# Performance work log

Measured on AMD Instinct MI355X. Metric: run time of the kernel, lower is better.

Reference implementation:

```python
import jax, jax.numpy as jnp
import numpy as np

N, E, G = 50000, 800000, 500
F_IN, H_DIM, L, NH, HD, OUT = 74, 256, 4, 8, 32, 1
SLOPE, EPS = 0.2, 1e-5


def setup_inputs() -> dict:
    key = jax.random.key(0)
    ks = jax.random.split(key, 24)
    rn = lambda k, s, sc: jax.random.normal(k, s, jnp.float32) * sc
    inp = {
        "x": jax.random.normal(ks[0], (N, F_IN), jnp.float32),
        "edge_index": jax.random.randint(ks[1], (2, E), 0, N),
        "batch": jnp.sort(jax.random.randint(ks[2], (N,), 0, G)),
        "in_w": rn(ks[3], (F_IN, H_DIM), 1.0 / np.sqrt(F_IN)),
        "in_b": jnp.zeros((H_DIM,), jnp.float32),
        "wl": rn(ks[4], (L, H_DIM, H_DIM), 1.0 / np.sqrt(H_DIM)),
        "wl_b": jnp.zeros((L, H_DIM), jnp.float32),
        "wr": rn(ks[5], (L, H_DIM, H_DIM), 1.0 / np.sqrt(H_DIM)),
        "wr_b": jnp.zeros((L, H_DIM), jnp.float32),
        "att": rn(ks[6], (L, NH, HD), 1.0 / np.sqrt(HD)),
        "gat_b": jnp.zeros((L, H_DIM), jnp.float32),
        "ln_g": jnp.ones((L, H_DIM), jnp.float32),
        "ln_b": jnp.zeros((L, H_DIM), jnp.float32),
        "out_w": rn(ks[7], (H_DIM, H_DIM), 1.0 / np.sqrt(H_DIM)),
        "out_b": jnp.zeros((H_DIM,), jnp.float32),
        "p1_w": rn(ks[8], (H_DIM, H_DIM // 2), 1.0 / np.sqrt(H_DIM)),
        "p1_b": jnp.zeros((H_DIM // 2,), jnp.float32),
        "bn1_g": jnp.ones((H_DIM // 2,), jnp.float32),
        "bn1_b": jnp.zeros((H_DIM // 2,), jnp.float32),
        "p2_w": rn(ks[9], (H_DIM // 2, H_DIM // 4), 1.0 / np.sqrt(H_DIM // 2)),
        "p2_b": jnp.zeros((H_DIM // 4,), jnp.float32),
        "bn2_g": jnp.ones((H_DIM // 4,), jnp.float32),
        "bn2_b": jnp.zeros((H_DIM // 4,), jnp.float32),
        "p3_w": rn(ks[10], (H_DIM // 4, OUT), 1.0 / np.sqrt(H_DIM // 4)),
        "p3_b": jnp.zeros((OUT,), jnp.float32),
    }
    return inp


def _layer_norm(x, g, b):
    m = x.mean(-1, keepdims=True)
    v = ((x - m) ** 2).mean(-1, keepdims=True)
    return (x - m) * jax.lax.rsqrt(v + EPS) * g + b


def _batch_norm(x, g, b):
    m = x.mean(0)
    v = ((x - m) ** 2).mean(0)
    return (x - m) * jax.lax.rsqrt(v + EPS) * g + b


def _gatv2(h, src, dst, wl, wl_b, wr, wr_b, att, bias, n):
    xl = (h @ wl + wl_b).reshape(n, NH, HD)  # source transform
    xr = (h @ wr + wr_b).reshape(n, NH, HD)  # target transform
    e = jax.nn.leaky_relu(xl[src] + xr[dst], SLOPE)      # [E, H, D]
    score = jnp.einsum('ehd,hd->eh', e, att)             # [E, H]
    smax = jax.ops.segment_max(score, dst, num_segments=n)
    num = jnp.exp(score - smax[dst])
    den = jax.ops.segment_sum(num, dst, num_segments=n)
    alpha = num / (den[dst] + 1e-16)                     # segment softmax per dst
    out = jax.ops.segment_sum(xl[src] * alpha[:, :, None], dst, num_segments=n)
    return out.reshape(n, NH * HD) + bias


def reference(x, edge_index, batch, in_w, in_b, wl, wl_b, wr, wr_b, att, gat_b,
              ln_g, ln_b, out_w, out_b, p1_w, p1_b, bn1_g, bn1_b,
              p2_w, p2_b, bn2_g, bn2_b, p3_w, p3_b):
    n = x.shape[0]
    loops = jnp.arange(n)
    src = jnp.concatenate([edge_index[0], loops])  # add self-loops (PyG default)
    dst = jnp.concatenate([edge_index[1], loops])
    h = x @ in_w + in_b
    for i in range(L):
        res = h
        g = _gatv2(h, src, dst, wl[i], wl_b[i], wr[i], wr_b[i], att[i], gat_b[i], n)
        if i > 0:
            g = g + res
        h = jax.nn.relu(_layer_norm(g, ln_g[i], ln_b[i]))
    h = h @ out_w + out_b
    cnt = jax.ops.segment_sum(jnp.ones((n,), h.dtype), batch, num_segments=G)
    gr = jax.ops.segment_sum(h, batch, num_segments=G) / jnp.maximum(cnt, 1.0)[:, None]
    z = jax.nn.relu(_batch_norm(gr @ p1_w + p1_b, bn1_g, bn1_b))
    z = jax.nn.relu(_batch_norm(z @ p2_w + p2_b, bn2_g, bn2_b))
    return z @ p3_w + p3_b
```

## Files before the change

kernel.cpp:

```cpp
#include <hip/hip_runtime.h>
#include <hip/hip_bf16.h>

#define F_IN   74
#define HDIM   256
#define NHEAD  8
#define HEADD  32
#define NLAYER 4
#define SLOPE  0.2f
#define EPSN   1e-5f

typedef __attribute__((ext_vector_type(8))) short bf16x8;
typedef __attribute__((ext_vector_type(4))) float f32x4;

__device__ __forceinline__ float bf2f(unsigned short u){
  union { unsigned int i; float f; } x; x.i = ((unsigned int)u) << 16; return x.f;
}
__device__ __forceinline__ unsigned short f2bf(float f){
  union { float f; unsigned int i; } x; x.f = f;
  unsigned int u = x.i;
  return (unsigned short)((u + 0x7FFFu + ((u >> 16) & 1u)) >> 16);
}

#define GLOAD16(g, s) __builtin_amdgcn_global_load_lds( \
  (const __attribute__((address_space(1))) void*)(g), \
  (__attribute__((address_space(3))) void*)(s), 16, 0, 0)

__global__ void k_hist(const int* __restrict__ dst, int* __restrict__ deg, int e){
  int i = blockIdx.x * 256 + threadIdx.x;
  if (i < e) atomicAdd(&deg[dst[i]], 1);
}

__global__ __launch_bounds__(256) void k_scan1(const int* __restrict__ deg,
    int* __restrict__ rowp, int* __restrict__ bsum, int n){
  __shared__ int wsum[4];
  const int tid = threadIdx.x, lane = tid & 63, wid = tid >> 6;
  const int i = blockIdx.x * 256 + tid;
  int v = (i < n) ? (deg[i] + 1) : 0;
  int xv = v;
  #pragma unroll
  for (int off = 1; off < 64; off <<= 1){
    int t = __shfl_up(xv, off);
    if (lane >= off) xv += t;
  }
  if (lane == 63) wsum[wid] = xv;
  __syncthreads();
  int woff = 0, total = 0;
  #pragma unroll
  for (int w = 0; w < 4; ++w){
    int s = wsum[w];
    total += s;
    if (w < wid) woff += s;
  }
  if (i < n) rowp[i] = woff + xv - v;
  if (tid == 0) bsum[blockIdx.x] = total;
}
__global__ __launch_bounds__(256) void k_scan2(const int* __restrict__ bsum,
    int* __restrict__ boff, int nb){
  __shared__ int wsum[4];
  const int tid = threadIdx.x, lane = tid & 63, wid = tid >> 6;
  int v = (tid < nb) ? bsum[tid] : 0;
  int xv = v;
  #pragma unroll
  for (int off = 1; off < 64; off <<= 1){
    int t = __shfl_up(xv, off);
    if (lane >= off) xv += t;
  }
  if (lane == 63) wsum[wid] = xv;
  __syncthreads();
  int woff = 0, total = 0;
  #pragma unroll
  for (int w = 0; w < 4; ++w){
    int s = wsum[w];
    total += s;
    if (w < wid) woff += s;
  }
  if (tid <= nb) boff[tid] = woff + xv - v;
  if (tid == 0) boff[nb] = total;
}
__global__ void k_scan3(int* __restrict__ rowp, const int* __restrict__ boff,
                        int n, int nb){
  int i = blockIdx.x * 256 + threadIdx.x;
  if (i < n) rowp[i] += boff[blockIdx.x];
  if (i == 0) rowp[n] = boff[nb];
}

__global__ void k_copy(const int* __restrict__ a, int* __restrict__ b, int n){
  int i = blockIdx.x * 256 + threadIdx.x;
  if (i < n) b[i] = a[i];
}
__global__ void k_fill(const int* __restrict__ src, const int* __restrict__ dst,
                       int* __restrict__ cur, int* __restrict__ csr, int e){
  int i = blockIdx.x * 256 + threadIdx.x;
  if (i < e){
    int p = atomicAdd(&cur[dst[i]], 1);
    csr[p] = src[i];
  }
}
__global__ void k_fillself(int* __restrict__ cur, int* __restrict__ csr, int n){
  int i = blockIdx.x * 256 + threadIdx.x;
  if (i < n){
    int p = atomicAdd(&cur[i], 1);
    csr[p] = i;
  }
}

__global__ __launch_bounds__(256) void k_inproj(
    const float* __restrict__ x, const float* __restrict__ w,
    const float* __restrict__ b, unsigned short* __restrict__ h, int n)
{
  __shared__ float xs[32 * F_IN];
  const int n0 = blockIdx.x * 32;
  const int tid = threadIdx.x;
  const int maxidx = n * F_IN;
  for (int idx = tid; idx < 32 * F_IN; idx += 256){
    int gidx = n0 * F_IN + idx;
    xs[idx] = (gidx < maxidx) ? x[gidx] : 0.f;
  }
  __syncthreads();
  float acc[32];
  #pragma unroll
  for (int i = 0; i < 32; ++i) acc[i] = 0.f;
  for (int k = 0; k < F_IN; ++k){
    float wk = w[k * HDIM + tid];
    #pragma unroll
    for (int i = 0; i < 32; ++i) acc[i] += xs[i * F_IN + k] * wk;
  }
  float bb = b[tid];
  #pragma unroll
  for (int i = 0; i < 32; ++i){
    int r = n0 + i;
    if (r < n) h[(size_t)r * HDIM + tid] = f2bf(acc[i] + bb);
  }
}

__global__ __launch_bounds__(256) void k_wconv(const float* __restrict__ W,
    unsigned short* __restrict__ Wt, size_t mat_stride){
  __shared__ float tile[32][33];
  const int mat = blockIdx.z;
  const float* Wm = W + (size_t)mat * HDIM * HDIM;
  unsigned short* Wo = Wt + (size_t)mat * mat_stride;
  const int c0 = blockIdx.x * 32, r0 = blockIdx.y * 32;
  const int tx = threadIdx.x & 31, ty = threadIdx.x >> 5;
  #pragma unroll
  for (int i = 0; i < 32; i += 8)
    tile[ty + i][tx] = Wm[(size_t)(r0 + ty + i) * HDIM + c0 + tx];
  __syncthreads();
  #pragma unroll
  for (int i = 0; i < 32; i += 8)
    Wo[(size_t)(c0 + ty + i) * HDIM + r0 + tx] = f2bf(tile[tx][ty + i]);
}

__global__ void k_bcat(const float* __restrict__ wl_b, const float* __restrict__ wr_b,
                       float* __restrict__ bc){
  int i = blockIdx.x * 256 + threadIdx.x;
  if (i >= NLAYER * 512) return;
  int layer = i >> 9, c = i & 511;
  bc[i] = (c < 256) ? wl_b[layer * 256 + c] : wr_b[layer * 256 + (c - 256)];
}

__global__ __launch_bounds__(256) void k_gemm_mfma(
    const unsigned short* __restrict__ A, const unsigned short* __restrict__ Wt,
    const float* __restrict__ bias, unsigned short* __restrict__ C, int M, int ldc)
{
  __shared__ unsigned short As[2][128 * 64];
  __shared__ unsigned short Bs[2][128 * 64];
  const int tid = threadIdx.x;
  const int l   = tid & 63;
  const int w   = tid >> 6;
  const int wm  = w >> 1, wn = w & 1;
  const int row0 = blockIdx.x * 128;
  const int col0 = blockIdx.y * 128;

  const int srow   = l >> 3;
  const int schunk = l & 7;

  f32x4 acc[4][4];
  #pragma unroll
  for (int i = 0; i < 4; ++i)
    #pragma unroll
    for (int j = 0; j < 4; ++j) acc[i][j] = (f32x4){0.f, 0.f, 0.f, 0.f};

  auto stage = [&](int buf, int k0){
    #pragma unroll
    for (int i = 0; i < 4; ++i){
      const int rloc = w * 32 + i * 8 + srow;
      const int sw   = (schunk ^ (rloc & 7)) * 16;
      int ra = row0 + rloc; if (ra > M - 1) ra = M - 1;
      const char* srcA = (const char*)(A + (size_t)ra * HDIM + k0) + sw;
      GLOAD16(srcA, &As[buf][(w * 32 + i * 8) * 64]);
      const char* srcB = (const char*)(Wt + (size_t)(col0 + rloc) * HDIM + k0) + sw;
      GLOAD16(srcB, &Bs[buf][(w * 32 + i * 8) * 64]);
    }
  };

  auto compute = [&](int buf){
    #pragma unroll
    for (int kk = 0; kk < 2; ++kk){
      bf16x8 af[4], bfr[4];
      #pragma unroll
      for (int mi = 0; mi < 4; ++mi){
        const int row = wm * 64 + mi * 16 + (l & 15);
        const int t   = (kk * 4 + (l >> 4)) ^ (row & 7);
        af[mi] = *(const bf16x8*)((const char*)&As[buf][0] + row * 128 + t * 16);
      }
      #pragma unroll
      for (int ni = 0; ni < 4; ++ni){
        const int nn = wn * 64 + ni * 16 + (l & 15);
        const int t  = (kk * 4 + (l >> 4)) ^ (nn & 7);
        bfr[ni] = *(const bf16x8*)((const char*)&Bs[buf][0] + nn * 128 + t * 16);
      }
      #pragma unroll
      for (int mi = 0; mi < 4; ++mi)
        #pragma unroll
        for (int ni = 0; ni < 4; ++ni)
          acc[mi][ni] = __builtin_amdgcn_mfma_f32_16x16x32_bf16(
              af[mi], bfr[ni], acc[mi][ni], 0, 0, 0);
    }
  };

  stage(0, 0);
  int cur = 0;
  #pragma unroll
  for (int t = 0; t < 4; ++t){
    if (t < 3){
      stage(cur ^ 1, (t + 1) * 64);
      asm volatile("s_waitcnt vmcnt(8)" ::: "memory");
    } else {
      asm volatile("s_waitcnt vmcnt(0)" ::: "memory");
    }
    __builtin_amdgcn_s_barrier();
    compute(cur);
    asm volatile("" ::: "memory");
    __builtin_amdgcn_s_barrier();
    cur ^= 1;
  }

  #pragma unroll
  for (int mi = 0; mi < 4; ++mi){
    #pragma unroll
    for (int ni = 0; ni < 4; ++ni){
      const int col = col0 + wn * 64 + ni * 16 + (l & 15);
      const float bv = bias[col];
      #pragma unroll
      for (int r = 0; r < 4; ++r){
        const int row = row0 + wm * 64 + mi * 16 + (l >> 4) * 4 + r;
        if (row < M) C[(size_t)row * ldc + col] = f2bf(acc[mi][ni][r] + bv);
      }
    }
  }
}

__global__ __launch_bounds__(256) void k_gat(
    const unsigned short* __restrict__ xlr,
    const int* __restrict__ rp, const int* __restrict__ csr,
    const float* __restrict__ att, const float* __restrict__ gb,
    const float* __restrict__ lg, const float* __restrict__ lb,
    const unsigned short* __restrict__ hold, unsigned short* __restrict__ hnew,
    int n, int use_res)
{
  const int node = blockIdx.x * 4 + (threadIdx.x >> 6);
  if (node >= n) return;
  const int lane = threadIdx.x & 63;
  const int elem = lane << 2;
  const int head = lane >> 3;
  float4 attv = *(const float4*)(att + head * HEADD + (elem & 31));
  ushort4 ur = *(const ushort4*)(xlr + (size_t)node * 512 + 256 + elem);
  const float xr0 = bf2f(ur.x), xr1 = bf2f(ur.y), xr2 = bf2f(ur.z), xr3 = bf2f(ur.w);

  auto scoref = [&](ushort4 u)->float{
    float t0 = bf2f(u.x) + xr0; t0 = t0 > 0.f ? t0 : SLOPE * t0;
    float t1 = bf2f(u.y) + xr1; t1 = t1 > 0.f ? t1 : SLOPE * t1;
    float t2 = bf2f(u.z) + xr2; t2 = t2 > 0.f ? t2 : SLOPE * t2;
    float t3 = bf2f(u.w) + xr3; t3 = t3 > 0.f ? t3 : SLOPE * t3;
    float p = attv.x * t0 + attv.y * t1 + attv.z * t2 + attv.w * t3;
    p += __shfl_xor(p, 1);
    p += __shfl_xor(p, 2);
    p += __shfl_xor(p, 4);
    return p;
  };

  float m = -1e30f, l = 0.f, a0 = 0.f, a1 = 0.f, a2 = 0.f, a3 = 0.f;
  const int e0 = rp[node], e1 = rp[node + 1];
  int e = e0;
  for (; e + 4 <= e1; e += 4){
    int s0 = csr[e], s1 = csr[e + 1], s2 = csr[e + 2], s3 = csr[e + 3];
    ushort4 u0 = *(const ushort4*)(xlr + (size_t)s0 * 512 + elem);
    ushort4 u1 = *(const ushort4*)(xlr + (size_t)s1 * 512 + elem);
    ushort4 u2 = *(const ushort4*)(xlr + (size_t)s2 * 512 + elem);
    ushort4 u3 = *(const ushort4*)(xlr + (size_t)s3 * 512 + elem);
    float p0 = scoref(u0), p1 = scoref(u1), p2 = scoref(u2), p3 = scoref(u3);
    float mn = fmaxf(m, fmaxf(fmaxf(p0, p1), fmaxf(p2, p3)));
    float sc = __expf(m - mn);
    float q0 = __expf(p0 - mn), q1 = __expf(p1 - mn);
    float q2 = __expf(p2 - mn), q3 = __expf(p3 - mn);
    l = l * sc + q0 + q1 + q2 + q3;
    a0 = a0 * sc + q0 * bf2f(u0.x) + q1 * bf2f(u1.x) + q2 * bf2f(u2.x) + q3 * bf2f(u3.x);
    a1 = a1 * sc + q0 * bf2f(u0.y) + q1 * bf2f(u1.y) + q2 * bf2f(u2.y) + q3 * bf2f(u3.y);
    a2 = a2 * sc + q0 * bf2f(u0.z) + q1 * bf2f(u1.z) + q2 * bf2f(u2.z) + q3 * bf2f(u3.z);
    a3 = a3 * sc + q0 * bf2f(u0.w) + q1 * bf2f(u1.w) + q2 * bf2f(u2.w) + q3 * bf2f(u3.w);
    m = mn;
  }
  for (; e < e1; ++e){
    int s = csr[e];
    ushort4 u = *(const ushort4*)(xlr + (size_t)s * 512 + elem);
    float p = scoref(u);
    float mn = fmaxf(m, p);
    float sc = __expf(m - mn);
    float pe = __expf(p - mn);
    l  = l * sc + pe;
    a0 = a0 * sc + pe * bf2f(u.x);
    a1 = a1 * sc + pe * bf2f(u.y);
    a2 = a2 * sc + pe * bf2f(u.z);
    a3 = a3 * sc + pe * bf2f(u.w);
    m = mn;
  }
  const float inv = 1.f / l;
  const size_t base = (size_t)node * HDIM + elem;
  float f0 = a0 * inv + gb[elem + 0];
  float f1 = a1 * inv + gb[elem + 1];
  float f2 = a2 * inv + gb[elem + 2];
  float f3 = a3 * inv + gb[elem + 3];
  if (use_res){
    ushort4 hv = *(const ushort4*)(hold + base);
    f0 += bf2f(hv.x); f1 += bf2f(hv.y); f2 += bf2f(hv.z); f3 += bf2f(hv.w);
  }
  float s = f0 + f1 + f2 + f3;
  #pragma unroll
  for (int off = 1; off < 64; off <<= 1) s += __shfl_xor(s, off);
  const float mean = s * (1.f / HDIM);
  float d0 = f0 - mean, d1 = f1 - mean, d2 = f2 - mean, d3 = f3 - mean;
  float q = d0 * d0 + d1 * d1 + d2 * d2 + d3 * d3;
  #pragma unroll
  for (int off = 1; off < 64; off <<= 1) q += __shfl_xor(q, off);
  const float rs = rsqrtf(q * (1.f / HDIM) + EPSN);
  float o0 = d0 * rs * lg[elem + 0] + lb[elem + 0]; o0 = o0 > 0.f ? o0 : 0.f;
  float o1 = d1 * rs * lg[elem + 1] + lb[elem + 1]; o1 = o1 > 0.f ? o1 : 0.f;
  float o2 = d2 * rs * lg[elem + 2] + lb[elem + 2]; o2 = o2 > 0.f ? o2 : 0.f;
  float o3 = d3 * rs * lg[elem + 3] + lb[elem + 3]; o3 = o3 > 0.f ? o3 : 0.f;
  ushort4 st; st.x = f2bf(o0); st.y = f2bf(o1); st.z = f2bf(o2); st.w = f2bf(o3);
  *(ushort4*)(hnew + base) = st;
}

__global__ __launch_bounds__(256) void k_pool2(
    const unsigned short* __restrict__ ho, const int* __restrict__ batch,
    float* __restrict__ gr, int n)
{
  const int g = blockIdx.x;
  int lo = 0, hi = n;
  while (lo < hi){ int mid = (lo + hi) >> 1; if (batch[mid] < g) lo = mid + 1; else hi = mid; }
  const int s = lo;
  hi = n;
  while (lo < hi){ int mid = (lo + hi) >> 1; if (batch[mid] < g + 1) lo = mid + 1; else hi = mid; }
  const int e = lo;
  const int j = threadIdx.x;
  float acc = 0.f;
  for (int i = s; i < e; ++i) acc += bf2f(ho[(size_t)i * HDIM + j]);
  int c = e - s; if (c < 1) c = 1;
  gr[(size_t)g * HDIM + j] = acc / (float)c;
}

__global__ void k_fc(const float* __restrict__ in, const float* __restrict__ w,
                     const float* __restrict__ b, float* __restrict__ out,
                     int kin, int kout){
  __shared__ float s[256];
  int g = blockIdx.x, j = threadIdx.x;
  for (int k = j; k < kin; k += blockDim.x) s[k] = in[(size_t)g * kin + k];
  __syncthreads();
  float a = b[j];
  for (int k = 0; k < kin; ++k) a = fmaf(s[k], w[k * kout + j], a);
  out[(size_t)g * kout + j] = a;
}
__global__ __launch_bounds__(256) void k_bnstats(const float* __restrict__ z,
    float* __restrict__ mean, float* __restrict__ rstd, int g_, int c_){
  int c = blockIdx.x;
  float s = 0.f, s2 = 0.f;
  for (int r = threadIdx.x; r < g_; r += 256){
    float v = z[(size_t)r * c_ + c];
    s += v; s2 += v * v;
  }
  #pragma unroll
  for (int off = 1; off < 64; off <<= 1){ s += __shfl_xor(s, off); s2 += __shfl_xor(s2, off); }
  __shared__ float sw[4], sw2[4];
  int lane = threadIdx.x & 63, wid = threadIdx.x >> 6;
  if (lane == 0){ sw[wid] = s; sw2[wid] = s2; }
  __syncthreads();
  if (threadIdx.x == 0){
    float ts = sw[0] + sw[1] + sw[2] + sw[3];
    float ts2 = sw2[0] + sw2[1] + sw2[2] + sw2[3];
    float mm = ts / g_;
    float vv = ts2 / g_ - mm * mm;
    mean[c] = mm; rstd[c] = rsqrtf(vv + EPSN);
  }
}
__global__ void k_bnrelu(float* __restrict__ z, const float* __restrict__ mean,
                         const float* __restrict__ rstd, const float* __restrict__ g,
                         const float* __restrict__ b, int total, int c_){
  int i = blockIdx.x * 256 + threadIdx.x;
  if (i < total){
    int c = i & (c_ - 1);
    float v = (z[i] - mean[c]) * rstd[c] * g[c] + b[c];
    z[i] = v > 0.f ? v : 0.f;
  }
}
__global__ __launch_bounds__(256) void k_out(const float* __restrict__ z,
    const float* __restrict__ w, const float* __restrict__ b,
    float* __restrict__ out, int g_){
  int g = blockIdx.x * 4 + (threadIdx.x >> 6);
  if (g >= g_) return;
  int lane = threadIdx.x & 63;
  float v = z[(size_t)g * 64 + lane] * w[lane];
  #pragma unroll
  for (int off = 1; off < 64; off <<= 1) v += __shfl_xor(v, off);
  if (lane == 0) out[g] = v + b[0];
}

extern "C" void kernel_launch(void* const* d_in, const int* in_sizes, int n_in,
                              void* d_out, int out_size, void* d_ws, size_t ws_size,
                              hipStream_t stream)
{
  const float* x     = (const float*)d_in[0];
  const int*   ei    = (const int*)  d_in[1];
  const int*   batch = (const int*)  d_in[2];
  const float* in_w  = (const float*)d_in[3];
  const float* in_b  = (const float*)d_in[4];
  const float* wl    = (const float*)d_in[5];
  const float* wl_b  = (const float*)d_in[6];
  const float* wr    = (const float*)d_in[7];
  const float* wr_b  = (const float*)d_in[8];
  const float* att   = (const float*)d_in[9];
  const float* gat_b = (const float*)d_in[10];
  const float* ln_g  = (const float*)d_in[11];
  const float* ln_b  = (const float*)d_in[12];
  const float* out_w = (const float*)d_in[13];
  const float* out_b = (const float*)d_in[14];
  const float* p1_w  = (const float*)d_in[15];
  const float* p1_b  = (const float*)d_in[16];
  const float* bn1_g = (const float*)d_in[17];
  const float* bn1_b = (const float*)d_in[18];
  const float* p2_w  = (const float*)d_in[19];
  const float* p2_b  = (const float*)d_in[20];
  const float* bn2_g = (const float*)d_in[21];
  const float* bn2_b = (const float*)d_in[22];
  const float* p3_w  = (const float*)d_in[23];
  const float* p3_b  = (const float*)d_in[24];

  const int n = in_sizes[0] / F_IN;
  const int e = in_sizes[1] / 2;
  const int g = out_size;
  const int nb = (n + 255) / 256;

  char* p = (char*)d_ws;
  auto take = [&](size_t bytes)->char*{
    char* q = p; p += ((bytes + 255) & ~(size_t)255); return q;
  };
  unsigned short* hA   = (unsigned short*)take((size_t)n * HDIM * 2);
  unsigned short* hB   = (unsigned short*)take((size_t)n * HDIM * 2);
  unsigned short* xlr  = (unsigned short*)take((size_t)n * 512 * 2);
  unsigned short* WtLR = (unsigned short*)take((size_t)NLAYER * 512 * HDIM * 2);
  unsigned short* WtO  = (unsigned short*)take((size_t)HDIM * HDIM * 2);
  float* bconc = (float*)take((size_t)NLAYER * 512 * 4);
  int*   deg   = (int*)take((size_t)n * 4);
  int*   rowp  = (int*)take((size_t)(n + 1) * 4);
  int*   cur   = (int*)take((size_t)n * 4);
  int*   csr   = (int*)take((size_t)(e + n) * 4);
  int*   bsum  = (int*)take((size_t)(nb + 1) * 4);
  int*   boff  = (int*)take((size_t)(nb + 1) * 4);
  float* gr    = (float*)take((size_t)g * HDIM * 4);
  float* z1    = (float*)take((size_t)g * 128 * 4);
  float* z2    = (float*)take((size_t)g * 64 * 4);
  float* mean1 = (float*)take(128 * 4);
  float* rstd1 = (float*)take(128 * 4);
  float* mean2 = (float*)take(64 * 4);
  float* rstd2 = (float*)take(64 * 4);
  (void)ws_size; (void)n_in;

  hipMemsetAsync(deg, 0, (size_t)n * 4, stream);
  k_hist<<<(e + 255) / 256, 256, 0, stream>>>(ei + e, deg, e);
  k_scan1<<<nb, 256, 0, stream>>>(deg, rowp, bsum, n);
  k_scan2<<<1, 256, 0, stream>>>(bsum, boff, nb);
  k_scan3<<<nb, 256, 0, stream>>>(rowp, boff, n, nb);
  k_copy<<<(n + 255) / 256, 256, 0, stream>>>(rowp, cur, n);
  k_fill<<<(e + 255) / 256, 256, 0, stream>>>(ei, ei + e, cur, csr, e);
  k_fillself<<<(n + 255) / 256, 256, 0, stream>>>(cur, csr, n);

  k_wconv<<<dim3(8, 8, 4), 256, 0, stream>>>(wl, WtLR, (size_t)512 * HDIM);
  k_wconv<<<dim3(8, 8, 4), 256, 0, stream>>>(wr, WtLR + (size_t)256 * HDIM, (size_t)512 * HDIM);
  k_wconv<<<dim3(8, 8, 1), 256, 0, stream>>>(out_w, WtO, (size_t)HDIM * HDIM);
  k_bcat<<<(NLAYER * 512 + 255) / 256, 256, 0, stream>>>(wl_b, wr_b, bconc);

  k_inproj<<<(n + 31) / 32, 256, 0, stream>>>(x, in_w, in_b, hA, n);

  unsigned short* hcur = hA;
  unsigned short* hnext = hB;
  for (int i = 0; i < NLAYER; ++i){
    k_gemm_mfma<<<dim3((n + 127) / 128, 4), 256, 0, stream>>>(
        hcur, WtLR + (size_t)i * 512 * HDIM, bconc + i * 512, xlr, n, 512);
    k_gat<<<(n + 3) / 4, 256, 0, stream>>>(xlr, rowp, csr,
        att + (size_t)i * NHEAD * HEADD, gat_b + i * HDIM,
        ln_g + i * HDIM, ln_b + i * HDIM, hcur, hnext, n, i > 0 ? 1 : 0);
    unsigned short* t = hcur; hcur = hnext; hnext = t;
  }
  k_gemm_mfma<<<dim3((n + 127) / 128, 2), 256, 0, stream>>>(
      hcur, WtO, out_b, hnext, n, HDIM);

  k_pool2<<<g, 256, 0, stream>>>(hnext, batch, gr, n);

  k_fc<<<g, 128, 0, stream>>>(gr, p1_w, p1_b, z1, HDIM, 128);
  k_bnstats<<<128, 256, 0, stream>>>(z1, mean1, rstd1, g, 128);
  k_bnrelu<<<(g * 128 + 255) / 256, 256, 0, stream>>>(z1, mean1, rstd1, bn1_g, bn1_b, g * 128, 128);
  k_fc<<<g, 64, 0, stream>>>(z1, p2_w, p2_b, z2, 128, 64);
  k_bnstats<<<64, 256, 0, stream>>>(z2, mean2, rstd2, g, 64);
  k_bnrelu<<<(g * 64 + 255) / 256, 256, 0, stream>>>(z2, mean2, rstd2, bn2_g, bn2_b, g * 64, 64);
  k_out<<<(g + 3) / 4, 256, 0, stream>>>(z2, p3_w, p3_b, (float*)d_out, g);
}
```

Baseline: 758.0 us.

## Use MFMA for input projection, drop softmax max tracking, fuse scan copy

The input projection now runs on bf16 MFMA instructions. The input and weight are first converted to bf16 and padded to K=96, with the padded input stored in the xlr scratch buffer. The GAT aggregation drops the online-softmax running maximum and rescaling and just accumulates exp(score), which saves several exp and multiply operations per edge. That risks overflow when scores are large. The separate k_copy of rowp into cur is folded into k_scan3, removing one launch.

```diff
diff --git a/kernel.cpp b/kernel.cpp
--- a/kernel.cpp
+++ b/kernel.cpp
@@ -2,6 +2,7 @@
 #include <hip/hip_bf16.h>
 
 #define F_IN   74
+#define KPAD   96
 #define HDIM   256
 #define NHEAD  8
 #define HEADD  32
@@ -77,17 +78,17 @@
   if (tid <= nb) boff[tid] = woff + xv - v;
   if (tid == 0) boff[nb] = total;
 }
-__global__ void k_scan3(int* __restrict__ rowp, const int* __restrict__ boff,
-                        int n, int nb){
+__global__ void k_scan3(int* __restrict__ rowp, int* __restrict__ cur,
+                        const int* __restrict__ boff, int n, int nb){
   int i = blockIdx.x * 256 + threadIdx.x;
-  if (i < n) rowp[i] += boff[blockIdx.x];
+  if (i < n){
+    int v = rowp[i] + boff[blockIdx.x];
+    rowp[i] = v;
+    cur[i] = v;
+  }
   if (i == 0) rowp[n] = boff[nb];
 }
 
-__global__ void k_copy(const int* __restrict__ a, int* __restrict__ b, int n){
-  int i = blockIdx.x * 256 + threadIdx.x;
-  if (i < n) b[i] = a[i];
-}
 __global__ void k_fill(const int* __restrict__ src, const int* __restrict__ dst,
                        int* __restrict__ cur, int* __restrict__ csr, int e){
   int i = blockIdx.x * 256 + threadIdx.x;
@@ -104,32 +105,77 @@
   }
 }
 
-__global__ __launch_bounds__(256) void k_inproj(
-    const float* __restrict__ x, const float* __restrict__ w,
-    const float* __restrict__ b, unsigned short* __restrict__ h, int n)
+__global__ void k_xconv(const float* __restrict__ x, unsigned short* __restrict__ xb,
+                        int n){
+  int idx = blockIdx.x * 256 + threadIdx.x;
+  int total = n * KPAD;
+  if (idx >= total) return;
+  int row = idx / KPAD;
+  int k = idx - row * KPAD;
+  float v = (k < F_IN) ? x[(size_t)row * F_IN + k] : 0.f;
+  xb[idx] = f2bf(v);
+}
+
+__global__ void k_wconv_in(const float* __restrict__ w, unsigned short* __restrict__ Wt){
+  int idx = blockIdx.x * 256 + threadIdx.x;
+  if (idx >= HDIM * KPAD) return;
+  int c = idx / KPAD;
+  int k = idx - c * KPAD;
+  float v = (k < F_IN) ? w[(size_t)k * HDIM + c] : 0.f;
+  Wt[idx] = f2bf(v);
+}
+
+__global__ __launch_bounds__(256) void k_inproj_mfma(
+    const unsigned short* __restrict__ xb, const unsigned short* __restrict__ Wt,
+    const float* __restrict__ bias, unsigned short* __restrict__ C, int M)
 {
-  __shared__ float xs[32 * F_IN];
-  const int n0 = blockIdx.x * 32;
-  const int tid = threadIdx.x;
-  const int maxidx = n * F_IN;
-  for (int idx = tid; idx < 32 * F_IN; idx += 256){
-    int gidx = n0 * F_IN + idx;
-    xs[idx] = (gidx < maxidx) ? x[gidx] : 0.f;
-  }
-  __syncthreads();
-  float acc[32];
-  #pragma unroll
-  for (int i = 0; i < 32; ++i) acc[i] = 0.f;
-  for (int k = 0; k < F_IN; ++k){
-    float wk = w[k * HDIM + tid];
-    #pragma unroll
-    for (int i = 0; i < 32; ++i) acc[i] += xs[i * F_IN + k] * wk;
-  }
-  float bb = b[tid];
-  #pragma unroll
-  for (int i = 0; i < 32; ++i){
-    int r = n0 + i;
-    if (r < n) h[(size_t)r * HDIM + tid] = f2bf(acc[i] + bb);
+  const int l = threadIdx.x & 63;
+  const int w = threadIdx.x >> 6;
+  const int wm = w >> 1, wn = w & 1;
+  const int row0 = blockIdx.x * 128;
+  const int col0 = blockIdx.y * 128;
+
+  f32x4 acc[4][4];
+  #pragma unroll
+  for (int i = 0; i < 4; ++i)
+    #pragma unroll
+    for (int j = 0; j < 4; ++j) acc[i][j] = (f32x4){0.f, 0.f, 0.f, 0.f};
+
+  #pragma unroll
+  for (int kk = 0; kk < 3; ++kk){
+    const int kof = kk * 32 + (l >> 4) * 8;
+    bf16x8 af[4], bfr[4];
+    #pragma unroll
+    for (int mi = 0; mi < 4; ++mi){
+      int row = row0 + wm * 64 + mi * 16 + (l & 15);
+      if (row > M - 1) row = M - 1;
+      af[mi] = *(const bf16x8*)(xb + (size_t)row * KPAD + kof);
+    }
+    #pragma unroll
+    for (int ni = 0; ni < 4; ++ni){
+      const int col = col0 + wn * 64 + ni * 16 + (l & 15);
+      bfr[ni] = *(const bf16x8*)(Wt + (size_t)col * KPAD + kof);
+    }
+    #pragma unroll
+    for (int mi = 0; mi < 4; ++mi)
+      #pragma unroll
+      for (int ni = 0; ni < 4; ++ni)
+        acc[mi][ni] = __builtin_amdgcn_mfma_f32_16x16x32_bf16(
+            af[mi], bfr[ni], acc[mi][ni], 0, 0, 0);
+  }
+
+  #pragma unroll
+  for (int mi = 0; mi < 4; ++mi){
+    #pragma unroll
+    for (int ni = 0; ni < 4; ++ni){
+      const int col = col0 + wn * 64 + ni * 16 + (l & 15);
+      const float bv = bias[col];
+      #pragma unroll
+      for (int r = 0; r < 4; ++r){
+        const int row = row0 + wm * 64 + mi * 16 + (l >> 4) * 4 + r;
+        if (row < M) C[(size_t)row * HDIM + col] = f2bf(acc[mi][ni][r] + bv);
+      }
+    }
   }
 }
 
@@ -279,7 +325,7 @@
     return p;
   };
 
-  float m = -1e30f, l = 0.f, a0 = 0.f, a1 = 0.f, a2 = 0.f, a3 = 0.f;
+  float l = 0.f, a0 = 0.f, a1 = 0.f, a2 = 0.f, a3 = 0.f;
   const int e0 = rp[node], e1 = rp[node + 1];
   int e = e0;
   for (; e + 4 <= e1; e += 4){
@@ -288,31 +334,23 @@
     ushort4 u1 = *(const ushort4*)(xlr + (size_t)s1 * 512 + elem);
     ushort4 u2 = *(const ushort4*)(xlr + (size_t)s2 * 512 + elem);
     ushort4 u3 = *(const ushort4*)(xlr + (size_t)s3 * 512 + elem);
-    float p0 = scoref(u0), p1 = scoref(u1), p2 = scoref(u2), p3 = scoref(u3);
-    float mn = fmaxf(m, fmaxf(fmaxf(p0, p1), fmaxf(p2, p3)));
-    float sc = __expf(m - mn);
-    float q0 = __expf(p0 - mn), q1 = __expf(p1 - mn);
-    float q2 = __expf(p2 - mn), q3 = __expf(p3 - mn);
-    l = l * sc + q0 + q1 + q2 + q3;
-    a0 = a0 * sc + q0 * bf2f(u0.x) + q1 * bf2f(u1.x) + q2 * bf2f(u2.x) + q3 * bf2f(u3.x);
-    a1 = a1 * sc + q0 * bf2f(u0.y) + q1 * bf2f(u1.y) + q2 * bf2f(u2.y) + q3 * bf2f(u3.y);
-    a2 = a2 * sc + q0 * bf2f(u0.z) + q1 * bf2f(u1.z) + q2 * bf2f(u2.z) + q3 * bf2f(u3.z);
-    a3 = a3 * sc + q0 * bf2f(u0.w) + q1 * bf2f(u1.w) + q2 * bf2f(u2.w) + q3 * bf2f(u3.w);
-    m = mn;
+    float q0 = __expf(scoref(u0)), q1 = __expf(scoref(u1));
+    float q2 = __expf(scoref(u2)), q3 = __expf(scoref(u3));
+    l += q0 + q1 + q2 + q3;
+    a0 += q0 * bf2f(u0.x) + q1 * bf2f(u1.x) + q2 * bf2f(u2.x) + q3 * bf2f(u3.x);
+    a1 += q0 * bf2f(u0.y) + q1 * bf2f(u1.y) + q2 * bf2f(u2.y) + q3 * bf2f(u3.y);
+    a2 += q0 * bf2f(u0.z) + q1 * bf2f(u1.z) + q2 * bf2f(u2.z) + q3 * bf2f(u3.z);
+    a3 += q0 * bf2f(u0.w) + q1 * bf2f(u1.w) + q2 * bf2f(u2.w) + q3 * bf2f(u3.w);
   }
   for (; e < e1; ++e){
     int s = csr[e];
     ushort4 u = *(const ushort4*)(xlr + (size_t)s * 512 + elem);
-    float p = scoref(u);
-    float mn = fmaxf(m, p);
-    float sc = __expf(m - mn);
-    float pe = __expf(p - mn);
-    l  = l * sc + pe;
-    a0 = a0 * sc + pe * bf2f(u.x);
-    a1 = a1 * sc + pe * bf2f(u.y);
-    a2 = a2 * sc + pe * bf2f(u.z);
-    a3 = a3 * sc + pe * bf2f(u.w);
-    m = mn;
+    float q = __expf(scoref(u));
+    l  += q;
+    a0 += q * bf2f(u.x);
+    a1 += q * bf2f(u.y);
+    a2 += q * bf2f(u.z);
+    a3 += q * bf2f(u.w);
   }
   const float inv = 1.f / l;
   const size_t base = (size_t)node * HDIM + elem;
@@ -458,6 +496,7 @@
   unsigned short* xlr  = (unsigned short*)take((size_t)n * 512 * 2);
   unsigned short* WtLR = (unsigned short*)take((size_t)NLAYER * 512 * HDIM * 2);
   unsigned short* WtO  = (unsigned short*)take((size_t)HDIM * HDIM * 2);
+  unsigned short* WtI  = (unsigned short*)take((size_t)HDIM * KPAD * 2);
   float* bconc = (float*)take((size_t)NLAYER * 512 * 4);
   int*   deg   = (int*)take((size_t)n * 4);
   int*   rowp  = (int*)take((size_t)(n + 1) * 4);
@@ -472,23 +511,25 @@
   float* rstd1 = (float*)take(128 * 4);
   float* mean2 = (float*)take(64 * 4);
   float* rstd2 = (float*)take(64 * 4);
+  unsigned short* xb = xlr;
   (void)ws_size; (void)n_in;
 
   hipMemsetAsync(deg, 0, (size_t)n * 4, stream);
   k_hist<<<(e + 255) / 256, 256, 0, stream>>>(ei + e, deg, e);
   k_scan1<<<nb, 256, 0, stream>>>(deg, rowp, bsum, n);
   k_scan2<<<1, 256, 0, stream>>>(bsum, boff, nb);
-  k_scan3<<<nb, 256, 0, stream>>>(rowp, boff, n, nb);
-  k_copy<<<(n + 255) / 256, 256, 0, stream>>>(rowp, cur, n);
+  k_scan3<<<nb, 256, 0, stream>>>(rowp, cur, boff, n, nb);
   k_fill<<<(e + 255) / 256, 256, 0, stream>>>(ei, ei + e, cur, csr, e);
   k_fillself<<<(n + 255) / 256, 256, 0, stream>>>(cur, csr, n);
 
   k_wconv<<<dim3(8, 8, 4), 256, 0, stream>>>(wl, WtLR, (size_t)512 * HDIM);
   k_wconv<<<dim3(8, 8, 4), 256, 0, stream>>>(wr, WtLR + (size_t)256 * HDIM, (size_t)512 * HDIM);
   k_wconv<<<dim3(8, 8, 1), 256, 0, stream>>>(out_w, WtO, (size_t)HDIM * HDIM);
+  k_wconv_in<<<(HDIM * KPAD + 255) / 256, 256, 0, stream>>>(in_w, WtI);
   k_bcat<<<(NLAYER * 512 + 255) / 256, 256, 0, stream>>>(wl_b, wr_b, bconc);
 
-  k_inproj<<<(n + 31) / 32, 256, 0, stream>>>(x, in_w, in_b, hA, n);
+  k_xconv<<<((n * KPAD) + 255) / 256, 256, 0, stream>>>(x, xb, n);
+  k_inproj_mfma<<<dim3((n + 127) / 128, 2), 256, 0, stream>>>(xb, WtI, in_b, hA, n);
 
   unsigned short* hcur = hA;
   unsigned short* hnext = hB;
```

After: 707.6 us. 1.07x faster.
